# Performance work log

Hardware: AMD Instinct MI355X
Metric: run time of the kernel (lower is better)

## Reference

```python
import jax, jax.numpy as jnp
import numpy as np

B, H, L = 1024, 32, 3
D_S, D_ID = 512, 128
D_STEER = 3 * D_S + D_ID  # 1664
D_HID = 2048
HS, DQ = 16, 64
HDQ = HS * DQ  # 1024


def setup_inputs() -> dict:
    key = jax.random.key(0)
    ks = jax.random.split(key, 18)
    n = lambda k, shape, std: jax.random.normal(k, shape, dtype=jnp.float32) * std
    inp = {
        "x": jax.random.normal(ks[0], (B * H, D_STEER), dtype=jnp.float32),
        "id_in": jax.random.normal(ks[1], (B * H, D_ID), dtype=jnp.float32),
        # per-head content MLP params
        "in_proj_w": n(ks[2], (H, D_STEER, D_S), 0.014),
        "in_proj_b": jnp.zeros((H, D_S), jnp.float32),
        "norm_w": jnp.ones((H, L, D_S), jnp.float32),
        "up_w": n(ks[3], (H, L, D_S, D_HID), 0.014),
        "up_b": jnp.zeros((H, L, D_HID), jnp.float32),
        "down_w": n(ks[4], (H, L, D_HID, D_S), (2.0 / D_HID) ** 0.5),
        "down_b": jnp.zeros((H, L, D_S), jnp.float32),
        # q_proj: Linear(D_steer, 2*HDQ) -> GELU -> Linear(2*HDQ, HDQ)
        "q1_w": n(ks[5], (D_STEER, 2 * HDQ), 0.014),
        "q1_b": jnp.zeros((2 * HDQ,), jnp.float32),
        "q2_w": n(ks[6], (2 * HDQ, HDQ), 0.02),
        "q2_b": jnp.zeros((HDQ,), jnp.float32),
        # k_proj: Linear(D_id, 2*HDQ) -> GELU -> Linear(2*HDQ, HDQ)
        "k1_w": n(ks[7], (D_ID, 2 * HDQ), 0.014),
        "k1_b": jnp.zeros((2 * HDQ,), jnp.float32),
        "k2_w": n(ks[8], (2 * HDQ, HDQ), 0.02),
        "k2_b": jnp.zeros((HDQ,), jnp.float32),
    }
    return inp


def _per_head_mlp(x, in_proj_w, in_proj_b, norm_w, up_w, up_b, down_w, down_b):
    # x: [B*H, D_steer] -> [B*H, D_s]
    bh = x.shape[0]
    b = bh // H
    xh = x.reshape(b, H, D_STEER)
    h = jnp.einsum("bhd,hde->bhe", xh, in_proj_w) + in_proj_b[None]
    for i in range(norm_w.shape[1]):
        rms = jax.lax.rsqrt(jnp.mean(h * h, axis=-1, keepdims=True) + 1e-6)
        xn = h * rms * norm_w[:, i][None]
        hid = jax.nn.gelu(jnp.einsum("bhd,hde->bhe", xn, up_w[:, i]) + up_b[:, i][None], approximate=False)
        h = h + jnp.einsum("bhd,hde->bhe", hid, down_w[:, i]) + down_b[:, i][None]
    return h.reshape(bh, D_S)


def reference(x, id_in, in_proj_w, in_proj_b, norm_w, up_w, up_b, down_w, down_b,
              q1_w, q1_b, q2_w, q2_b, k1_w, k1_b, k2_w, k2_b):
    content = _per_head_mlp(x, in_proj_w, in_proj_b, norm_w, up_w, up_b, down_w, down_b)
    q = jax.nn.gelu(x @ q1_w + q1_b, approximate=False) @ q2_w + q2_b
    k = jax.nn.gelu(id_in @ k1_w + k1_b, approximate=False) @ k2_w + k2_b
    # concat outputs: [B*H, D_s + HDQ + HDQ]
    return jnp.concatenate([content, q, k], axis=-1)
```

## Files before the change

### kernel.cpp

```cpp
#include <hip/hip_runtime.h>
#include <hip/hip_bf16.h>
#include <math.h>

#define HH 32
#define LL 3
#define DS 512
#define DID 128
#define DSTEER 1664
#define DHID 2048
#define HDQ 1024
#define BHROWS 32768

typedef __attribute__((ext_vector_type(8))) short short8;
typedef __attribute__((ext_vector_type(4))) float f32x4;

typedef const __attribute__((address_space(1))) unsigned int* gptr_t;
typedef __attribute__((address_space(3))) unsigned int* lptr_t;

#define FENCE() asm volatile("" ::: "memory")
#define BAR() do { FENCE(); __builtin_amdgcn_s_barrier(); FENCE(); } while (0)
#define VMCNT4() asm volatile("s_waitcnt vmcnt(4)" ::: "memory")
#define VMCNT2() asm volatile("s_waitcnt vmcnt(2)" ::: "memory")
#define VMCNT0() asm volatile("s_waitcnt vmcnt(0)" ::: "memory")

__device__ __forceinline__ unsigned short f2bf(float f) {
  union { float f; unsigned int u; } x; x.f = f;
  unsigned int r = (x.u + 0x7FFFu + ((x.u >> 16) & 1u)) >> 16;
  return (unsigned short)r;
}
__device__ __forceinline__ unsigned int pk2(float a, float b) {
  return (unsigned int)f2bf(a) | ((unsigned int)f2bf(b) << 16);
}
__device__ __forceinline__ float gelu_exact(float v) {
  return 0.5f * v * (1.0f + erff(v * 0.70710678118654752440f));
}

__global__ void cvt_bf16_kernel(const float4* __restrict__ in, uint2* __restrict__ out, long n4) {
  long i = (long)blockIdx.x * blockDim.x + threadIdx.x;
  long stride = (long)gridDim.x * blockDim.x;
  for (; i < n4; i += stride) {
    float4 v = in[i];
    uint2 o; o.x = pk2(v.x, v.y); o.y = pk2(v.z, v.w);
    out[i] = o;
  }
}

__global__ void transpose_cvt_kernel(const float* __restrict__ in, long long in_bstride,
                                     unsigned short* __restrict__ out, long long out_bstride,
                                     int R, int C) {
  __shared__ float t[64][33];
  const int r0 = blockIdx.y * 32;
  const int c0 = blockIdx.x * 64;
  const float* bin = in + (long long)blockIdx.z * in_bstride;
  unsigned short* bout = out + (long long)blockIdx.z * out_bstride;
  const int tid = threadIdx.x;
  const int col = tid & 63, rr = tid >> 6;
  #pragma unroll
  for (int j = 0; j < 8; j++) {
    int r = j * 4 + rr;
    t[col][r] = bin[(size_t)(r0 + r) * C + c0 + col];
  }
  __syncthreads();
  const int rq = (tid & 7) * 4;
  const int cc = tid >> 3;
  #pragma unroll
  for (int j = 0; j < 2; j++) {
    int c = j * 32 + cc;
    float v0 = t[c][rq], v1 = t[c][rq + 1], v2 = t[c][rq + 2], v3 = t[c][rq + 3];
    uint2 o; o.x = pk2(v0, v1); o.y = pk2(v2, v3);
    *(uint2*)&bout[(size_t)(c0 + c) * R + r0 + rq] = o;
  }
}

__global__ void rms_scale_kernel(const float* __restrict__ h,
                                 const float* __restrict__ norm_w,
                                 unsigned short* __restrict__ xn, int layer) {
  int gw = (int)((blockIdx.x * blockDim.x + threadIdx.x) >> 6);
  int lane = threadIdx.x & 63;
  if (gw >= BHROWS) return;
  int head = gw & (HH - 1);
  const float4* hr = (const float4*)(h + (size_t)gw * DS);
  float4 v0 = hr[lane * 2], v1 = hr[lane * 2 + 1];
  float ss = v0.x*v0.x + v0.y*v0.y + v0.z*v0.z + v0.w*v0.w
           + v1.x*v1.x + v1.y*v1.y + v1.z*v1.z + v1.w*v1.w;
  #pragma unroll
  for (int off = 32; off > 0; off >>= 1) ss += __shfl_xor(ss, off, 64);
  float r = rsqrtf(ss * (1.0f / DS) + 1e-6f);
  const float4* nw = (const float4*)(norm_w + ((size_t)head * LL + layer) * DS);
  float4 w0 = nw[lane * 2], w1 = nw[lane * 2 + 1];
  uint4 o;
  o.x = pk2(v0.x * r * w0.x, v0.y * r * w0.y);
  o.y = pk2(v0.z * r * w0.z, v0.w * r * w0.w);
  o.z = pk2(v1.x * r * w1.x, v1.y * r * w1.y);
  o.w = pk2(v1.z * r * w1.z, v1.w * r * w1.w);
  *(uint4*)(xn + (size_t)gw * DS + (size_t)lane * 8) = o;
}

template<int EPI>
__global__ __launch_bounds__(512, 2)
void gemm256_kernel(const unsigned short* __restrict__ A, int lda, int rstep,
                    const unsigned short* __restrict__ Bt, int ldb, long long b_hstride,
                    const float* __restrict__ bias, int bias_hstride,
                    const float* __restrict__ resid, int ldr,
                    void* __restrict__ Cv, int ldc, int K) {
  __shared__ unsigned short lds[2 * 2 * 256 * 64];
  const int tid = threadIdx.x;
  const int lane = tid & 63;
  const int wave = tid >> 6;
  const int wr = wave >> 2, wc = wave & 3;
  const int head = blockIdx.z;
  const int gx = gridDim.x;
  const int nwg = gx * gridDim.y;
  int wgid = blockIdx.y * gx + blockIdx.x;
  { int cpx = nwg >> 3; wgid = (wgid & 7) * cpx + (wgid >> 3); }
  const int tn = wgid % gx, tm = wgid / gx;

  const int l3 = lane >> 3;
  const int gslot = ((lane & 7) ^ l3) * 8;
  const int mbase = wave * 8 + l3;
  const int nbase = (wave >> 2) * 64 + (wave & 3) * 8 + l3;
  const unsigned short* pA = A + ((size_t)(tm * 256 + mbase) * rstep + head) * lda + gslot;
  const unsigned short* pB = Bt + (size_t)head * b_hstride
                               + (size_t)(tn * 256 + nbase) * ldb + gslot;
  const size_t aBlk = (size_t)64 * rstep * lda;

  const int physk0 = ((lane >> 4) ^ (lane & 7)) * 8;
  const int physk1 = ((4 + (lane >> 4)) ^ (lane & 7)) * 8;
  const int aRow = wr * 128 + (lane & 15);
  const int bRow = wc * 32 + (lane & 15);

  auto stageA = [&](unsigned short* dstA, int h, size_t kels) {
    #pragma unroll
    for (int i = 0; i < 2; ++i)
      __builtin_amdgcn_global_load_lds(
          (gptr_t)(pA + (size_t)(i * 2 + h) * aBlk + kels),
          (lptr_t)(dstA + ((i * 2 + h) * 64 + wave * 8) * 64), 16, 0, 0);
  };
  auto stageB = [&](unsigned short* dstB, int h, size_t kels) {
    #pragma unroll
    for (int i = 0; i < 2; ++i)
      __builtin_amdgcn_global_load_lds(
          (gptr_t)(pB + (size_t)(i * 128 + h * 32) * ldb + kels),
          (lptr_t)(dstB + (h * 128 + i * 64 + wave * 8) * 64), 16, 0, 0);
  };

  f32x4 acc[8][4];
  #pragma unroll
  for (int i = 0; i < 8; ++i)
    #pragma unroll
    for (int j = 0; j < 4; ++j) acc[i][j] = (f32x4){0.f, 0.f, 0.f, 0.f};
  short8 a[4][2], b[4][2];

  stageA(lds, 0, 0);
  stageB(lds + 16384, 0, 0);
  stageB(lds + 16384, 1, 0);
  stageA(lds, 1, 0);
  VMCNT4();
  BAR();

  const int T = K >> 6;
  for (int t = 0; t < T; ++t) {
    unsigned short* rA = lds + (t & 1) * 32768;
    unsigned short* rB = rA + 16384;
    unsigned short* wA = lds + ((t + 1) & 1) * 32768;
    unsigned short* wB = wA + 16384;
    const size_t kn = (size_t)(t + 1) * 64;
    const bool more = (t + 1 < T);

    #pragma unroll
    for (int i = 0; i < 4; ++i) {
      a[i][0] = *(const short8*)&rA[(aRow + i * 16) * 64 + physk0];
      a[i][1] = *(const short8*)&rA[(aRow + i * 16) * 64 + physk1];
    }
    #pragma unroll
    for (int j = 0; j < 2; ++j) {
      b[j][0] = *(const short8*)&rB[(bRow + j * 16) * 64 + physk0];
      b[j][1] = *(const short8*)&rB[(bRow + j * 16) * 64 + physk1];
    }
    if (more) stageA(wA, 0, kn);
    BAR();
    __builtin_amdgcn_s_setprio(1);
    #pragma unroll
    for (int i = 0; i < 4; ++i)
      #pragma unroll
      for (int j = 0; j < 2; ++j) {
        acc[i][j] = __builtin_amdgcn_mfma_f32_16x16x32_bf16(a[i][0], b[j][0], acc[i][j], 0, 0, 0);
        acc[i][j] = __builtin_amdgcn_mfma_f32_16x16x32_bf16(a[i][1], b[j][1], acc[i][j], 0, 0, 0);
      }
    __builtin_amdgcn_s_setprio(0);
    if (more) VMCNT4(); else VMCNT2();
    BAR();

    #pragma unroll
    for (int j = 0; j < 2; ++j) {
      b[2 + j][0] = *(const short8*)&rB[(128 + bRow + j * 16) * 64 + physk0];
      b[2 + j][1] = *(const short8*)&rB[(128 + bRow + j * 16) * 64 + physk1];
    }
    if (more) stageB(wB, 0, kn);
    BAR();
    __builtin_amdgcn_s_setprio(1);
    #pragma unroll
    for (int i = 0; i < 4; ++i)
      #pragma unroll
      for (int j = 0; j < 2; ++j) {
        acc[i][2 + j] = __builtin_amdgcn_mfma_f32_16x16x32_bf16(a[i][0], b[2 + j][0], acc[i][2 + j], 0, 0, 0);
        acc[i][2 + j] = __builtin_amdgcn_mfma_f32_16x16x32_bf16(a[i][1], b[2 + j][1], acc[i][2 + j], 0, 0, 0);
      }
    __builtin_amdgcn_s_setprio(0);
    if (more) VMCNT4(); else VMCNT0();
    BAR();

    #pragma unroll
    for (int i = 0; i < 4; ++i) {
      a[i][0] = *(const short8*)&rA[(aRow + (4 + i) * 16) * 64 + physk0];
      a[i][1] = *(const short8*)&rA[(aRow + (4 + i) * 16) * 64 + physk1];
    }
    if (more) stageB(wB, 1, kn);
    BAR();
    __builtin_amdgcn_s_setprio(1);
    #pragma unroll
    for (int i = 0; i < 4; ++i)
      #pragma unroll
      for (int j = 0; j < 2; ++j) {
        acc[4 + i][2 + j] = __builtin_amdgcn_mfma_f32_16x16x32_bf16(a[i][0], b[2 + j][0], acc[4 + i][2 + j], 0, 0, 0);
        acc[4 + i][2 + j] = __builtin_amdgcn_mfma_f32_16x16x32_bf16(a[i][1], b[2 + j][1], acc[4 + i][2 + j], 0, 0, 0);
      }
    __builtin_amdgcn_s_setprio(0);
    BAR();

    if (more) stageA(wA, 1, kn);
    BAR();
    __builtin_amdgcn_s_setprio(1);
    #pragma unroll
    for (int i = 0; i < 4; ++i)
      #pragma unroll
      for (int j = 0; j < 2; ++j) {
        acc[4 + i][j] = __builtin_amdgcn_mfma_f32_16x16x32_bf16(a[i][0], b[j][0], acc[4 + i][j], 0, 0, 0);
        acc[4 + i][j] = __builtin_amdgcn_mfma_f32_16x16x32_bf16(a[i][1], b[j][1], acc[4 + i][j], 0, 0, 0);
      }
    __builtin_amdgcn_s_setprio(0);
    if (more) VMCNT4();
    BAR();
  }

  const float* bptr = bias + (size_t)head * bias_hstride;
  #pragma unroll
  for (int i = 0; i < 8; ++i) {
    #pragma unroll
    for (int j = 0; j < 4; ++j) {
      #pragma unroll
      for (int r = 0; r < 4; ++r) {
        int rowt = wr * 128 + i * 16 + (lane >> 4) * 4 + r;
        int colt = wc * 64 + j * 16 + (lane & 15);
        int col = tn * 256 + colt;
        size_t crow = (size_t)(tm * 256 + rowt) * rstep + head;
        float v = acc[i][j][r] + bptr[col];
        if (EPI == 1) {
          ((unsigned short*)Cv)[crow * (size_t)ldc + col] = f2bf(gelu_exact(v));
        } else if (EPI == 2) {
          v += resid[crow * (size_t)ldr + col];
          ((float*)Cv)[crow * (size_t)ldc + col] = v;
        } else {
          ((float*)Cv)[crow * (size_t)ldc + col] = v;
        }
      }
    }
  }
}

extern "C" void kernel_launch(void* const* d_in, const int* in_sizes, int n_in,
                              void* d_out, int out_size, void* d_ws, size_t ws_size,
                              hipStream_t stream) {
  const float* x         = (const float*)d_in[0];
  const float* id_in     = (const float*)d_in[1];
  const float* in_proj_w = (const float*)d_in[2];
  const float* in_proj_b = (const float*)d_in[3];
  const float* norm_w    = (const float*)d_in[4];
  const float* up_w      = (const float*)d_in[5];
  const float* up_b      = (const float*)d_in[6];
  const float* down_w    = (const float*)d_in[7];
  const float* down_b    = (const float*)d_in[8];
  const float* q1_w      = (const float*)d_in[9];
  const float* q1_b      = (const float*)d_in[10];
  const float* q2_w      = (const float*)d_in[11];
  const float* q2_b      = (const float*)d_in[12];
  const float* k1_w      = (const float*)d_in[13];
  const float* k1_b      = (const float*)d_in[14];
  const float* k2_w      = (const float*)d_in[15];
  const float* k2_b      = (const float*)d_in[16];
  float* out = (float*)d_out;

  char* ws = (char*)d_ws;
  unsigned short* x_bf  = (unsigned short*)ws; ws += (size_t)BHROWS * DSTEER * 2;
  unsigned short* id_bf = (unsigned short*)ws; ws += (size_t)BHROWS * DID * 2;
  float*          hbuf  = (float*)ws;          ws += (size_t)BHROWS * DS * 4;
  unsigned short* xn    = (unsigned short*)ws; ws += (size_t)BHROWS * DS * 2;
  unsigned short* hid   = (unsigned short*)ws; ws += (size_t)BHROWS * DHID * 2;
  unsigned short* wbuf  = (unsigned short*)ws; ws += (size_t)HH * DHID * DS * 2;

  cvt_bf16_kernel<<<2048, 256, 0, stream>>>((const float4*)x, (uint2*)x_bf,
                                            (long)BHROWS * DSTEER / 4);
  cvt_bf16_kernel<<<512, 256, 0, stream>>>((const float4*)id_in, (uint2*)id_bf,
                                           (long)BHROWS * DID / 4);

  transpose_cvt_kernel<<<dim3(2 * HDQ / 64, DSTEER / 32, 1), 256, 0, stream>>>(
      q1_w, 0, wbuf, 0, DSTEER, 2 * HDQ);
  gemm256_kernel<1><<<dim3(8, 128, 1), 512, 0, stream>>>(
      x_bf, DSTEER, 1, wbuf, DSTEER, 0, q1_b, 0, nullptr, 0, hid, 2 * HDQ, DSTEER);
  transpose_cvt_kernel<<<dim3(HDQ / 64, 2 * HDQ / 32, 1), 256, 0, stream>>>(
      q2_w, 0, wbuf, 0, 2 * HDQ, HDQ);
  gemm256_kernel<0><<<dim3(4, 128, 1), 512, 0, stream>>>(
      hid, 2 * HDQ, 1, wbuf, 2 * HDQ, 0, q2_b, 0, nullptr, 0, out + 512, 2560, 2 * HDQ);

  transpose_cvt_kernel<<<dim3(2 * HDQ / 64, DID / 32, 1), 256, 0, stream>>>(
      k1_w, 0, wbuf, 0, DID, 2 * HDQ);
  gemm256_kernel<1><<<dim3(8, 128, 1), 512, 0, stream>>>(
      id_bf, DID, 1, wbuf, DID, 0, k1_b, 0, nullptr, 0, hid, 2 * HDQ, DID);
  transpose_cvt_kernel<<<dim3(HDQ / 64, 2 * HDQ / 32, 1), 256, 0, stream>>>(
      k2_w, 0, wbuf, 0, 2 * HDQ, HDQ);
  gemm256_kernel<0><<<dim3(4, 128, 1), 512, 0, stream>>>(
      hid, 2 * HDQ, 1, wbuf, 2 * HDQ, 0, k2_b, 0, nullptr, 0, out + 1536, 2560, 2 * HDQ);

  transpose_cvt_kernel<<<dim3(DS / 64, DSTEER / 32, HH), 256, 0, stream>>>(
      in_proj_w, (long long)DSTEER * DS, wbuf, (long long)DS * DSTEER, DSTEER, DS);
  gemm256_kernel<0><<<dim3(2, 4, 32), 512, 0, stream>>>(
      x_bf, DSTEER, HH, wbuf, DSTEER, (long long)DS * DSTEER, in_proj_b, DS,
      nullptr, 0, hbuf, DS, DSTEER);

  for (int i = 0; i < LL; i++) {
    rms_scale_kernel<<<8192, 256, 0, stream>>>(hbuf, norm_w, xn, i);
    transpose_cvt_kernel<<<dim3(DHID / 64, DS / 32, HH), 256, 0, stream>>>(
        up_w + (size_t)i * DS * DHID, (long long)LL * DS * DHID,
        wbuf, (long long)DHID * DS, DS, DHID);
    gemm256_kernel<1><<<dim3(8, 4, 32), 512, 0, stream>>>(
        xn, DS, HH, wbuf, DS, (long long)DHID * DS,
        up_b + (size_t)i * DHID, LL * DHID, nullptr, 0, hid, DHID, DS);
    transpose_cvt_kernel<<<dim3(DS / 64, DHID / 32, HH), 256, 0, stream>>>(
        down_w + (size_t)i * DHID * DS, (long long)LL * DHID * DS,
        wbuf, (long long)DS * DHID, DHID, DS);
    float* cout = (i < 2) ? hbuf : out;
    int ldc = (i < 2) ? DS : 2560;
    gemm256_kernel<2><<<dim3(2, 4, 32), 512, 0, stream>>>(
        hid, DHID, HH, wbuf, DHID, (long long)DS * DHID,
        down_b + (size_t)i * DS, LL * DS, hbuf, DS, cout, ldc, DHID);
  }
}
```

Baseline: 1.707 ms.

## Deepen GEMM global-to-LDS prefetch to two k-tiles ahead within double buffer

Restructures the GEMM mainloop so global loads for tile t+2 are issued into the current buffer's regions as soon as they are consumed, while the remaining part of tile t+1 is loaded early. The prologue now stages almost two tiles, and the vmcnt waits are rebalanced (10/8/2/0) so more loads stay in flight. The aim is to hide more global memory latency behind the MFMA work. The risk is that the wait counts or region reuse are subtly wrong, which would cause LDS races.

```diff
diff --git a/kernel.cpp b/kernel.cpp
--- a/kernel.cpp
+++ b/kernel.cpp
@@ -19,9 +19,10 @@
 
 #define FENCE() asm volatile("" ::: "memory")
 #define BAR() do { FENCE(); __builtin_amdgcn_s_barrier(); FENCE(); } while (0)
-#define VMCNT4() asm volatile("s_waitcnt vmcnt(4)" ::: "memory")
-#define VMCNT2() asm volatile("s_waitcnt vmcnt(2)" ::: "memory")
-#define VMCNT0() asm volatile("s_waitcnt vmcnt(0)" ::: "memory")
+#define VMCNT10() asm volatile("s_waitcnt vmcnt(10)" ::: "memory")
+#define VMCNT8()  asm volatile("s_waitcnt vmcnt(8)" ::: "memory")
+#define VMCNT2()  asm volatile("s_waitcnt vmcnt(2)" ::: "memory")
+#define VMCNT0()  asm volatile("s_waitcnt vmcnt(0)" ::: "memory")
 
 __device__ __forceinline__ unsigned short f2bf(float f) {
   union { float f; unsigned int u; } x; x.f = f;
@@ -151,21 +152,30 @@
     for (int j = 0; j < 4; ++j) acc[i][j] = (f32x4){0.f, 0.f, 0.f, 0.f};
   short8 a[4][2], b[4][2];
 
+  const int T = K >> 6;
   stageA(lds, 0, 0);
   stageB(lds + 16384, 0, 0);
   stageB(lds + 16384, 1, 0);
   stageA(lds, 1, 0);
-  VMCNT4();
+  if (1 < T) {
+    stageA(lds + 32768, 0, 64);
+    stageB(lds + 32768 + 16384, 0, 64);
+    stageB(lds + 32768 + 16384, 1, 64);
+    VMCNT8();
+  } else {
+    VMCNT2();
+  }
   BAR();
 
-  const int T = K >> 6;
   for (int t = 0; t < T; ++t) {
     unsigned short* rA = lds + (t & 1) * 32768;
     unsigned short* rB = rA + 16384;
-    unsigned short* wA = lds + ((t + 1) & 1) * 32768;
-    unsigned short* wB = wA + 16384;
-    const size_t kn = (size_t)(t + 1) * 64;
-    const bool more = (t + 1 < T);
+    unsigned short* nA = lds + ((t + 1) & 1) * 32768;
+    unsigned short* cA = rA;
+    unsigned short* cB = rB;
+    const size_t k1 = (size_t)(t + 1) * 64;
+    const size_t k2 = (size_t)(t + 2) * 64;
+    const bool m1 = (t + 1 < T), m2 = (t + 2 < T);
 
     #pragma unroll
     for (int i = 0; i < 4; ++i) {
@@ -177,7 +187,7 @@
       b[j][0] = *(const short8*)&rB[(bRow + j * 16) * 64 + physk0];
       b[j][1] = *(const short8*)&rB[(bRow + j * 16) * 64 + physk1];
     }
-    if (more) stageA(wA, 0, kn);
+    if (m1) stageA(nA, 1, k1);
     BAR();
     __builtin_amdgcn_s_setprio(1);
     #pragma unroll
@@ -188,7 +198,6 @@
         acc[i][j] = __builtin_amdgcn_mfma_f32_16x16x32_bf16(a[i][1], b[j][1], acc[i][j], 0, 0, 0);
       }
     __builtin_amdgcn_s_setprio(0);
-    if (more) VMCNT4(); else VMCNT2();
     BAR();
 
     #pragma unroll
@@ -196,7 +205,7 @@
       b[2 + j][0] = *(const short8*)&rB[(128 + bRow + j * 16) * 64 + physk0];
       b[2 + j][1] = *(const short8*)&rB[(128 + bRow + j * 16) * 64 + physk1];
     }
-    if (more) stageB(wB, 0, kn);
+    if (m2) stageA(cA, 0, k2);
     BAR();
     __builtin_amdgcn_s_setprio(1);
     #pragma unroll
@@ -207,7 +216,7 @@
         acc[i][2 + j] = __builtin_amdgcn_mfma_f32_16x16x32_bf16(a[i][1], b[2 + j][1], acc[i][2 + j], 0, 0, 0);
       }
     __builtin_amdgcn_s_setprio(0);
-    if (more) VMCNT4(); else VMCNT0();
+    if (m2) { VMCNT10(); } else if (m1) { VMCNT8(); } else { VMCNT0(); }
     BAR();
 
     #pragma unroll
@@ -215,7 +224,7 @@
       a[i][0] = *(const short8*)&rA[(aRow + (4 + i) * 16) * 64 + physk0];
       a[i][1] = *(const short8*)&rA[(aRow + (4 + i) * 16) * 64 + physk1];
     }
-    if (more) stageB(wB, 1, kn);
+    if (m2) stageB(cB, 0, k2);
     BAR();
     __builtin_amdgcn_s_setprio(1);
     #pragma unroll
@@ -228,7 +237,7 @@
     __builtin_amdgcn_s_setprio(0);
     BAR();
 
-    if (more) stageA(wA, 1, kn);
+    if (m2) stageB(cB, 1, k2);
     BAR();
     __builtin_amdgcn_s_setprio(1);
     #pragma unroll
@@ -239,7 +248,7 @@
         acc[4 + i][j] = __builtin_amdgcn_mfma_f32_16x16x32_bf16(a[i][1], b[j][1], acc[4 + i][j], 0, 0, 0);
       }
     __builtin_amdgcn_s_setprio(0);
-    if (more) VMCNT4();
+    if (m1) { if (m2) { VMCNT8(); } else { VMCNT2(); } }
     BAR();
   }
 
```

After: 1.726 ms. No clear change (+1.1%).
